# Kernel optimization log

Measured on AMD Instinct MI355X. Metric: run time of the kernel, lower is better.

The kernel has to match this reference:

```python
import jax, jax.numpy as jnp
import numpy as np

B, C, H, W = 16, 128, 64, 64
NH = 8
HD = C // NH          # head dim == pos_embed_dim
WIN = 5               # relative-position window
OUT = 512             # out_dim of the final 1x1 projection


def _dwconv(x, w, pad):
    """Depthwise 2D conv, x: (N, Cin, H, W), w: (Cin, 1, kh, kw)."""
    return jax.lax.conv_general_dilated(
        x, w, window_strides=(1, 1), padding=[(pad, pad), (pad, pad)],
        dimension_numbers=('NCHW', 'OIHW', 'NCHW'),
        feature_group_count=x.shape[1])


def setup_inputs() -> dict:
    key = jax.random.key(0)
    ks = jax.random.split(key, 6)
    src = jax.random.normal(ks[0], (B, C, H, W), jnp.float32)
    cpe_w = jax.random.normal(ks[1], (C, 1, 3, 3), jnp.float32) * 0.1
    qkv_w = jax.random.normal(ks[2], (3 * C, C), jnp.float32) * (1.0 / np.sqrt(C))
    rel_pos = jax.random.normal(ks[3], (HD, WIN, WIN), jnp.float32) * 0.02
    conv1d_w = jax.random.normal(ks[4], (3,), jnp.float32) * 0.5
    out_w = jax.random.normal(ks[5], (OUT, 2 * C), jnp.float32) * (1.0 / np.sqrt(2 * C))
    return dict(src=src, cpe_w=cpe_w, qkv_w=qkv_w, rel_pos=rel_pos,
                conv1d_w=conv1d_w, out_w=out_w)


def reference(src, cpe_w, qkv_w, rel_pos, conv1d_w, out_w):
    scaling = HD ** (-0.5)
    feature_raw = src

    # CPE: depthwise 3x3 conv residual
    s = _dwconv(src, cpe_w, 1) + src

    # 1x1 QKV conv == channel GEMM
    qkv = jnp.einsum('oc,bchw->bohw', qkv_w, s)          # (B, 3C, H, W)
    q, k, v = jnp.split(qkv, 3, axis=1)                  # each (B, C, H, W)

    q = q.reshape(B * NH, HD, H, W)
    k = k.reshape(B * NH, HD, H, W)
    v = v.reshape(B * NH, HD, H, W)

    N = H * W
    kf = jax.nn.softmax(k.reshape(B * NH, HD, N), axis=-1)   # softmax over spatial
    vf = v.reshape(B * NH, HD, N)
    content_lambda = jnp.einsum('bin,bon->bio', kf, vf)      # (B*NH, HD, HD)
    qf = q.reshape(B * NH, HD, N) * scaling
    content_output = jnp.einsum('bin,bio->bon', qf, content_lambda)
    content_output = content_output.reshape(B * NH, HD, H, W)

    # relative-position lambda: depthwise 5x5 conv of v with rel_pos_embed
    position_lambda = _dwconv(v, rel_pos[:, None, :, :], WIN // 2)
    position_output = q * position_lambda

    result1 = (content_output + position_output).reshape(B, C, H, W)

    # ECA-style channel attention on the raw input
    pool = jnp.mean(feature_raw, axis=(2, 3))                # (B, C)
    xp = jnp.pad(pool, ((0, 0), (1, 1)))
    ca = jax.nn.sigmoid(conv1d_w[0] * xp[:, :-2]
                        + conv1d_w[1] * xp[:, 1:-1]
                        + conv1d_w[2] * xp[:, 2:])           # (B, C)
    result2 = feature_raw * ca[:, :, None, None]

    cat = jnp.concatenate([result1, result2], axis=1)       # (B, 2C, H, W)
    return jnp.einsum('oc,bchw->bohw', out_w, cat)           # (B, OUT, H, W)
```

## Files before the change

### kernel.cpp

```cpp
#include <hip/hip_runtime.h>
#include <hip/hip_bf16.h>
#include <math.h>

#define Bb   16
#define Cc   128
#define Hh   64
#define Wwid 64
#define Nn   4096
#define NHh  8
#define HDd  16
#define BHh  128
#define TCc  384
#define OUTc 512
#define KK2  256

typedef _Float16 f16x8 __attribute__((ext_vector_type(8)));
typedef float    f32x4 __attribute__((ext_vector_type(4)));

__device__ __forceinline__ ushort f2h_bits(float f) {
    _Float16 h = (_Float16)f;
    ushort u;
    __builtin_memcpy(&u, &h, 2);
    return u;
}
__device__ __forceinline__ float h2f_bits(ushort u) {
    _Float16 h;
    __builtin_memcpy(&h, &u, 2);
    return (float)h;
}

__global__ void __launch_bounds__(256) cpe_cvt_kernel(
        const float* __restrict__ src, const float* __restrict__ cpe_w,
        const float* __restrict__ qkv_w, const float* __restrict__ out_w,
        ushort* __restrict__ s, float* __restrict__ pool,
        ushort* __restrict__ wq16, ushort* __restrict__ wo16) {
    int t = threadIdx.x;
    if (blockIdx.x >= 2048) {
        int i = (blockIdx.x - 2048) * 256 + t;
        const int na = TCc * Cc, nb = OUTc * KK2;
        if (i < na) wq16[i] = f2h_bits(qkv_w[i]);
        else if (i < na + nb) wo16[i - na] = f2h_bits(out_w[i - na]);
        return;
    }
    int bc = blockIdx.x;
    int c  = bc & (Cc - 1);
    const float* sp = src + (size_t)bc * Nn;
    __shared__ float pl[66 * 66];
    __shared__ float red[256];
    for (int i = t; i < 66 * 66; i += 256) pl[i] = 0.f;
    __syncthreads();
    float lsum = 0.f;
    for (int i = t; i < Nn / 4; i += 256) {
        float4 v4 = ((const float4*)sp)[i];
        lsum += v4.x + v4.y + v4.z + v4.w;
        int e = i * 4, y = e >> 6, x = e & 63;
        float* d = &pl[(y + 1) * 66 + x + 1];
        d[0] = v4.x; d[1] = v4.y; d[2] = v4.z; d[3] = v4.w;
    }
    red[t] = lsum;
    float w[9];
#pragma unroll
    for (int k = 0; k < 9; k++) w[k] = cpe_w[c * 9 + k];
    __syncthreads();
    for (int s2 = 128; s2 > 0; s2 >>= 1) {
        if (t < s2) red[t] += red[t + s2];
        __syncthreads();
    }
    if (t == 0) pool[bc] = red[0] * (1.0f / Nn);
    int x = t & 63, ys = (t >> 6) * 16;
    float r[3][3];
#pragma unroll
    for (int k = 0; k < 2; k++)
#pragma unroll
        for (int j = 0; j < 3; j++) r[k][j] = pl[(ys + k) * 66 + x + j];
    ushort* dst = s + (size_t)bc * Nn;
#pragma unroll
    for (int yy = 0; yy < 16; yy++) {
        int y = ys + yy;
#pragma unroll
        for (int j = 0; j < 3; j++) r[2][j] = pl[(y + 2) * 66 + x + j];
        float acc = r[1][1];
#pragma unroll
        for (int k = 0; k < 3; k++)
#pragma unroll
            for (int j = 0; j < 3; j++) acc += r[k][j] * w[k * 3 + j];
        dst[y * 64 + x] = f2h_bits(acc);
#pragma unroll
        for (int j = 0; j < 3; j++) { r[0][j] = r[1][j]; r[1][j] = r[2][j]; }
    }
}

__global__ void transpose_s(const ushort* __restrict__ s, ushort* __restrict__ sT) {
    int bz = blockIdx.z;
    int c0 = blockIdx.y * 64;
    int n0 = blockIdx.x * 64;
    __shared__ ushort t[64][68];
    int nn = threadIdx.x & 63, c4 = threadIdx.x >> 6;
    const ushort* sp = s + ((size_t)bz * Cc + c0) * Nn + n0;
#pragma unroll
    for (int p = 0; p < 16; p++) {
        int cc = p * 4 + c4;
        t[cc][nn] = sp[(size_t)cc * Nn + nn];
    }
    __syncthreads();
    int cw = threadIdx.x & 63, n4 = threadIdx.x >> 6;
    ushort* dp = sT + ((size_t)bz * Nn + n0) * Cc + c0;
#pragma unroll
    for (int p = 0; p < 16; p++) {
        int n = p * 4 + n4;
        dp[(size_t)n * Cc + cw] = t[cw][n];
    }
}

template<int K, int M, int MODE>
__global__ void __launch_bounds__(256) gemm_tn(const ushort* __restrict__ A,
                                               const ushort* __restrict__ Bt,
                                               float* __restrict__ C,
                                               ushort* __restrict__ q16,
                                               float* __restrict__ kf32,
                                               ushort* __restrict__ v16) {
    const int bz = blockIdx.z;
    const int m0 = blockIdx.y * 128;
    const int n0 = blockIdx.x * 128;
    __shared__ __align__(16) ushort Al[128 * 32];
    __shared__ __align__(16) ushort Bl[128 * 32];
    const int tid  = threadIdx.x;
    const int wave = tid >> 6, lane = tid & 63;
    const int r = lane & 15, q = lane >> 4;
    const int wr = wave >> 1, wc = wave & 1;

    const ushort* Ag = A + (size_t)m0 * K;
    const ushort* Bg = Bt + ((size_t)bz * Nn + n0) * K;

    f32x4 acc[4][4] = {};

    for (int k0 = 0; k0 < K; k0 += 32) {
#pragma unroll
        for (int p = 0; p < 2; p++) {
            int seg = p * 4 + wave;
            int idx = seg * 64 + lane;
            int row = idx >> 2, ch = idx & 3;
            const ushort* ga = Ag + (size_t)row * K + k0 + ch * 8;
            const ushort* gb = Bg + (size_t)row * K + k0 + ch * 8;
            __builtin_amdgcn_global_load_lds(
                (const __attribute__((address_space(1))) void*)(const void*)ga,
                (__attribute__((address_space(3))) void*)(void*)(Al + seg * 512),
                16, 0, 0);
            __builtin_amdgcn_global_load_lds(
                (const __attribute__((address_space(1))) void*)(const void*)gb,
                (__attribute__((address_space(3))) void*)(void*)(Bl + seg * 512),
                16, 0, 0);
        }
        __syncthreads();

        const ushort* Apt = Al + (size_t)(wr * 64 + r) * 32 + q * 8;
        const ushort* Bpt = Bl + (size_t)(wc * 64 + r) * 32 + q * 8;
        f16x8 af[4], bf[4];
#pragma unroll
        for (int i = 0; i < 4; i++) af[i] = *(const f16x8*)(Apt + i * 16 * 32);
#pragma unroll
        for (int j = 0; j < 4; j++) bf[j] = *(const f16x8*)(Bpt + j * 16 * 32);
#pragma unroll
        for (int i = 0; i < 4; i++)
#pragma unroll
            for (int j = 0; j < 4; j++)
                acc[i][j] = __builtin_amdgcn_mfma_f32_16x16x32_f16(af[i], bf[j], acc[i][j], 0, 0, 0);
        __syncthreads();
    }

    if constexpr (MODE == 0) {
        float* Cp = C + ((size_t)bz * M + m0 + wr * 64) * Nn + n0 + wc * 64;
#pragma unroll
        for (int i = 0; i < 4; i++)
#pragma unroll
            for (int j = 0; j < 4; j++)
#pragma unroll
                for (int e = 0; e < 4; e++)
                    Cp[(size_t)(i * 16 + q * 4 + e) * Nn + j * 16 + r] = acc[i][j][e];
    } else {
        size_t base = ((size_t)bz * Cc + wr * 64) * Nn + n0 + wc * 64;
        if (blockIdx.y == 1) {
            float* Cp = kf32 + base;
#pragma unroll
            for (int i = 0; i < 4; i++)
#pragma unroll
                for (int j = 0; j < 4; j++)
#pragma unroll
                    for (int e = 0; e < 4; e++)
                        Cp[(size_t)(i * 16 + q * 4 + e) * Nn + j * 16 + r] = acc[i][j][e];
        } else {
            ushort* Cp = (blockIdx.y == 0 ? q16 : v16) + base;
#pragma unroll
            for (int i = 0; i < 4; i++)
#pragma unroll
                for (int j = 0; j < 4; j++)
#pragma unroll
                    for (int e = 0; e < 4; e++)
                        Cp[(size_t)(i * 16 + q * 4 + e) * Nn + j * 16 + r] = f2h_bits(acc[i][j][e]);
        }
    }
}

__global__ void __launch_bounds__(256) lam_pos_kernel(
        const float* __restrict__ kf32, const ushort* __restrict__ v16,
        const float* __restrict__ rel,
        ushort* __restrict__ pos, float* __restrict__ lamP,
        float* __restrict__ lamE) {
    __shared__ float smem[68 * 68];
    int t = threadIdx.x;

    if (blockIdx.x >= 2048) {
        int bid2 = blockIdx.x - 2048;
        int bh   = bid2 >> 1;
        int half = bid2 & 1;
        int b = bh >> 3, h = bh & 7;
        int wave = t >> 6, lane = t & 63;
        int r = lane & 15, q = lane >> 4;
        const float*  kf = kf32 + ((size_t)b * Cc + h * HDd) * Nn;
        const ushort* vf = v16  + ((size_t)b * Cc + h * HDd) * Nn;

        f32x4 acc = {};
        float esum = 0.f;
        int nbase = half * 2048 + wave * 512;
#pragma unroll 4
        for (int s = 0; s < 16; s++) {
            int n = nbase + s * 32 + q * 8;
            float4 ka = *(const float4*)(kf + (size_t)r * Nn + n);
            float4 kb = *(const float4*)(kf + (size_t)r * Nn + n + 4);
            f16x8 bf = *(const f16x8*)(vf + (size_t)r * Nn + n);
            float e0 = __expf(ka.x), e1 = __expf(ka.y), e2 = __expf(ka.z), e3 = __expf(ka.w);
            float e4 = __expf(kb.x), e5 = __expf(kb.y), e6 = __expf(kb.z), e7 = __expf(kb.w);
            esum += (e0 + e1 + e2 + e3) + (e4 + e5 + e6 + e7);
            f16x8 af;
            af[0] = (_Float16)e0; af[1] = (_Float16)e1;
            af[2] = (_Float16)e2; af[3] = (_Float16)e3;
            af[4] = (_Float16)e4; af[5] = (_Float16)e5;
            af[6] = (_Float16)e6; af[7] = (_Float16)e7;
            acc = __builtin_amdgcn_mfma_f32_16x16x32_f16(af, bf, acc, 0, 0, 0);
        }

        float* red   = smem;
        float* esred = smem + 1024;
#pragma unroll
        for (int e = 0; e < 4; e++) red[wave * 256 + lane * 4 + e] = acc[e];
        esred[wave * 64 + lane] = esum;
        __syncthreads();
        if (wave == 0) {
#pragma unroll
            for (int e = 0; e < 4; e++) {
                float v = red[0 * 256 + lane * 4 + e] + red[1 * 256 + lane * 4 + e]
                        + red[2 * 256 + lane * 4 + e] + red[3 * 256 + lane * 4 + e];
                int row = q * 4 + e;
                lamP[(size_t)half * (BHh * 256) + bh * 256 + row * 16 + r] = v;
            }
            if (lane < 16) {
                float tot = 0.f;
#pragma unroll
                for (int w2 = 0; w2 < 4; w2++)
#pragma unroll
                    for (int qq = 0; qq < 4; qq++)
                        tot += esred[w2 * 64 + qq * 16 + lane];
                lamE[(size_t)half * (BHh * 16) + bh * 16 + lane] = tot;
            }
        }
        return;
    }

    int bc = blockIdx.x;
    int c = bc & (Cc - 1);
    const ushort* vp = v16 + (size_t)bc * Nn;
    float* pl = smem;
    for (int i = t; i < 68 * 68; i += 256) pl[i] = 0.f;
    __syncthreads();
    for (int i = t; i < Nn / 8; i += 256) {
        uint4 u = ((const uint4*)vp)[i];
        ushort us[8]; *(uint4*)us = u;
        int e = i * 8, y = e >> 6, x = e & 63;
        float* d = &pl[(y + 2) * 68 + x + 2];
#pragma unroll
        for (int j = 0; j < 8; j++) d[j] = h2f_bits(us[j]);
    }
    float w[25];
#pragma unroll
    for (int k = 0; k < 25; k++) w[k] = rel[(c & (HDd - 1)) * 25 + k];
    __syncthreads();
    int x = t & 63, ys = (t >> 6) * 16;
    float r[5][5];
#pragma unroll
    for (int k = 0; k < 4; k++)
#pragma unroll
        for (int j = 0; j < 5; j++) r[k][j] = pl[(ys + k) * 68 + x + j];
    ushort* dst = pos + (size_t)bc * Nn;
#pragma unroll
    for (int yy = 0; yy < 16; yy++) {
        int y = ys + yy;
#pragma unroll
        for (int j = 0; j < 5; j++) r[4][j] = pl[(y + 4) * 68 + x + j];
        float acc = 0.f;
#pragma unroll
        for (int k = 0; k < 5; k++)
#pragma unroll
            for (int j = 0; j < 5; j++) acc += r[k][j] * w[k * 5 + j];
        dst[y * 64 + x] = f2h_bits(acc);
#pragma unroll
        for (int k = 0; k < 4; k++)
#pragma unroll
            for (int j = 0; j < 5; j++) r[k][j] = r[k + 1][j];
    }
}

__global__ void __launch_bounds__(256) combine_eca_kernel(
        const ushort* __restrict__ q16, const float* __restrict__ lamP,
        const float* __restrict__ lamE, const ushort* __restrict__ pos,
        const float* __restrict__ src, const float* __restrict__ pool,
        const float* __restrict__ w3, ushort* __restrict__ catT) {
    __shared__ float smem[2240];
    int tid = threadIdx.x;

    if (blockIdx.x >= 2048) {
        int bid2 = blockIdx.x - 2048;
        int n0 = (bid2 & 63) * 64, c0 = ((bid2 >> 6) & 1) * 64, bz = bid2 >> 7;
        ushort* t = (ushort*)smem;
        float* ca_s = smem + 2176;
        if (tid < 64) {
            int c = c0 + tid;
            float left  = (c == 0)        ? 0.f : pool[bz * Cc + c - 1];
            float mid   = pool[bz * Cc + c];
            float right = (c == Cc - 1)   ? 0.f : pool[bz * Cc + c + 1];
            float v = w3[0] * left + w3[1] * mid + w3[2] * right;
            ca_s[tid] = 1.f / (1.f + __expf(-v));
        }
        __syncthreads();
        int nn = tid & 63, c4 = tid >> 6;
        const float* sp = src + ((size_t)bz * Cc + c0) * Nn + n0;
#pragma unroll
        for (int p = 0; p < 16; p++) {
            int cc = p * 4 + c4;
            t[cc * 68 + nn] = f2h_bits(sp[(size_t)cc * Nn + nn] * ca_s[cc]);
        }
        __syncthreads();
        int cw = tid & 63, n4 = tid >> 6;
        ushort* dp = catT + ((size_t)bz * Nn + n0) * KK2 + Cc + c0;
#pragma unroll
        for (int p = 0; p < 16; p++) {
            int n = p * 4 + n4;
            dp[(size_t)n * KK2 + cw] = t[cw * 68 + n];
        }
        return;
    }

    int bh   = blockIdx.x >> 4;
    int tile = blockIdx.x & 15;
    int n = tile * 256 + tid;
    int b = bh >> 3, h = bh & 7;
    float* lam_s = smem;
    {
        int i = tid >> 4;
        float es = lamE[bh * 16 + i] + lamE[(size_t)(BHh * 16) + bh * 16 + i];
        lam_s[tid] = (lamP[bh * 256 + tid]
                    + lamP[(size_t)(BHh * 256) + bh * 256 + tid]) / es;
    }
    __syncthreads();
    const ushort* qp = q16 + ((size_t)b * Cc + h * HDd) * Nn;
    float qv[16];
#pragma unroll
    for (int i = 0; i < 16; i++) qv[i] = h2f_bits(qp[(size_t)i * Nn + n]);
    const ushort* pp = pos + ((size_t)b * Cc + h * HDd) * Nn;
    float vals[16];
#pragma unroll
    for (int o = 0; o < 16; o++) {
        float co = 0.f;
#pragma unroll
        for (int i2 = 0; i2 < 16; i2++) co += qv[i2] * lam_s[i2 * 16 + o];
        vals[o] = co * 0.25f + qv[o] * h2f_bits(pp[(size_t)o * Nn + n]);
    }
    uint up[8];
#pragma unroll
    for (int o2 = 0; o2 < 8; o2++)
        up[o2] = (uint)f2h_bits(vals[2 * o2]) | ((uint)f2h_bits(vals[2 * o2 + 1]) << 16);
    uint4* dst = (uint4*)(catT + ((size_t)b * Nn + n) * KK2 + h * HDd);
    dst[0] = make_uint4(up[0], up[1], up[2], up[3]);
    dst[1] = make_uint4(up[4], up[5], up[6], up[7]);
}

extern "C" void kernel_launch(void* const* d_in, const int* in_sizes, int n_in,
                              void* d_out, int out_size, void* d_ws, size_t ws_size,
                              hipStream_t stream) {
    const float* src      = (const float*)d_in[0];
    const float* cpe_w    = (const float*)d_in[1];
    const float* qkv_w    = (const float*)d_in[2];
    const float* rel_pos  = (const float*)d_in[3];
    const float* conv1d_w = (const float*)d_in[4];
    const float* out_w    = (const float*)d_in[5];
    float* out = (float*)d_out;

    char* ws = (char*)d_ws;
    ushort* q16   = (ushort*)ws;                                 ws += (size_t)Bb * Cc * Nn * 2;
    float*  kf32  = (float*)ws;                                  ws += (size_t)Bb * Cc * Nn * 4;
    ushort* v16   = (ushort*)ws;                                 ws += (size_t)Bb * Cc * Nn * 2;
    ushort* pos   = (ushort*)ws;                                 ws += (size_t)Bb * Cc * Nn * 2;
    ushort* catT  = (ushort*)ws;                                 ws += (size_t)Bb * Nn * KK2 * 2;
    ushort* sT    = (ushort*)ws;                                 ws += (size_t)Bb * Nn * Cc * 2;
    ushort* s16   = (ushort*)catT;
    float*  lamP  = (float*)ws;                                  ws += (size_t)2 * BHh * 256 * 4;
    float*  lamE  = (float*)ws;                                  ws += (size_t)2 * BHh * 16 * 4;
    float*  pool  = (float*)ws;                                  ws += Bb * Cc * 4;
    ushort* wq16  = (ushort*)ws;                                 ws += (size_t)TCc * Cc * 2;
    ushort* wo16  = (ushort*)ws;                                 ws += (size_t)OUTc * KK2 * 2;

    {
        const int nw = TCc * Cc + OUTc * KK2;
        int cvt_blocks = (nw + 255) / 256;
        cpe_cvt_kernel<<<2048 + cvt_blocks, 256, 0, stream>>>(
            src, cpe_w, qkv_w, out_w, s16, pool, wq16, wo16);
    }
    {
        dim3 g(Nn / 64, Cc / 64, Bb);
        transpose_s<<<g, 256, 0, stream>>>(s16, sT);
    }
    {
        dim3 g(Nn / 128, TCc / 128, Bb);
        gemm_tn<Cc, TCc, 1><<<g, 256, 0, stream>>>(wq16, sT, nullptr, q16, kf32, v16);
    }
    lam_pos_kernel<<<2048 + 2 * BHh, 256, 0, stream>>>(kf32, v16, rel_pos, pos, lamP, lamE);
    combine_eca_kernel<<<2048 + 2048, 256, 0, stream>>>(
        q16, lamP, lamE, pos, src, pool, conv1d_w, catT);
    {
        dim3 g(Nn / 128, OUTc / 128, Bb);
        gemm_tn<KK2, OUTc, 0><<<g, 256, 0, stream>>>(wo16, catT, out, nullptr, nullptr, nullptr);
    }
}
```

Before: 268.3 us.

## Double-buffer GEMM LDS tiles, vectorize epilogue via LDS, cache fp16 src

The GEMM mainloop now uses two LDS buffers so the next K-slice is fetched while MFMAs run on the current one, which drops one barrier per iteration. Both GEMM epilogues stage accumulators through a per-wave LDS tile so global stores become float4 or packed-half vectors instead of scattered scalars. The CPE kernel also writes an fp16 copy of src, and the ECA branch reads that copy instead of re-reading fp32 src, which halves its read traffic. The cost is extra LDS per block (possible occupancy loss), an additional fp16 write pass of src, and slightly lower precision on the ECA path.

```diff
diff --git a/kernel.cpp b/kernel.cpp
--- a/kernel.cpp
+++ b/kernel.cpp
@@ -32,7 +32,8 @@
 __global__ void __launch_bounds__(256) cpe_cvt_kernel(
         const float* __restrict__ src, const float* __restrict__ cpe_w,
         const float* __restrict__ qkv_w, const float* __restrict__ out_w,
-        ushort* __restrict__ s, float* __restrict__ pool,
+        ushort* __restrict__ s, ushort* __restrict__ src16,
+        float* __restrict__ pool,
         ushort* __restrict__ wq16, ushort* __restrict__ wo16) {
     int t = threadIdx.x;
     if (blockIdx.x >= 2048) {
@@ -50,9 +51,13 @@
     for (int i = t; i < 66 * 66; i += 256) pl[i] = 0.f;
     __syncthreads();
     float lsum = 0.f;
+    ushort* s16p = src16 + (size_t)bc * Nn;
     for (int i = t; i < Nn / 4; i += 256) {
         float4 v4 = ((const float4*)sp)[i];
         lsum += v4.x + v4.y + v4.z + v4.w;
+        ushort4 h4 = make_ushort4(f2h_bits(v4.x), f2h_bits(v4.y),
+                                  f2h_bits(v4.z), f2h_bits(v4.w));
+        *(ushort4*)(s16p + i * 4) = h4;
         int e = i * 4, y = e >> 6, x = e & 63;
         float* d = &pl[(y + 1) * 66 + x + 1];
         d[0] = v4.x; d[1] = v4.y; d[2] = v4.z; d[3] = v4.w;
@@ -122,8 +127,9 @@
     const int bz = blockIdx.z;
     const int m0 = blockIdx.y * 128;
     const int n0 = blockIdx.x * 128;
-    __shared__ __align__(16) ushort Al[128 * 32];
-    __shared__ __align__(16) ushort Bl[128 * 32];
+    __shared__ __align__(16) ushort Al[2][128 * 32];
+    __shared__ __align__(16) ushort Bl[2][128 * 32];
+    __shared__ __align__(16) float  ep[4][16][66];
     const int tid  = threadIdx.x;
     const int wave = tid >> 6, lane = tid & 63;
     const int r = lane & 15, q = lane >> 4;
@@ -134,7 +140,7 @@
 
     f32x4 acc[4][4] = {};
 
-    for (int k0 = 0; k0 < K; k0 += 32) {
+    auto stage = [&](int buf, int k0) {
 #pragma unroll
         for (int p = 0; p < 2; p++) {
             int seg = p * 4 + wave;
@@ -144,17 +150,25 @@
             const ushort* gb = Bg + (size_t)row * K + k0 + ch * 8;
             __builtin_amdgcn_global_load_lds(
                 (const __attribute__((address_space(1))) void*)(const void*)ga,
-                (__attribute__((address_space(3))) void*)(void*)(Al + seg * 512),
+                (__attribute__((address_space(3))) void*)(void*)(&Al[buf][seg * 512]),
                 16, 0, 0);
             __builtin_amdgcn_global_load_lds(
                 (const __attribute__((address_space(1))) void*)(const void*)gb,
-                (__attribute__((address_space(3))) void*)(void*)(Bl + seg * 512),
+                (__attribute__((address_space(3))) void*)(void*)(&Bl[buf][seg * 512]),
                 16, 0, 0);
         }
-        __syncthreads();
-
-        const ushort* Apt = Al + (size_t)(wr * 64 + r) * 32 + q * 8;
-        const ushort* Bpt = Bl + (size_t)(wc * 64 + r) * 32 + q * 8;
+    };
+
+    constexpr int NT = K / 32;
+    stage(0, 0);
+    __syncthreads();
+#pragma unroll
+    for (int t = 0; t < NT; t++) {
+        const int cur = t & 1;
+        if (t + 1 < NT) stage(cur ^ 1, (t + 1) * 32);
+
+        const ushort* Apt = &Al[cur][(wr * 64 + r) * 32 + q * 8];
+        const ushort* Bpt = &Bl[cur][(wc * 64 + r) * 32 + q * 8];
         f16x8 af[4], bf[4];
 #pragma unroll
         for (int i = 0; i < 4; i++) af[i] = *(const f16x8*)(Apt + i * 16 * 32);
@@ -165,38 +179,62 @@
 #pragma unroll
             for (int j = 0; j < 4; j++)
                 acc[i][j] = __builtin_amdgcn_mfma_f32_16x16x32_f16(af[i], bf[j], acc[i][j], 0, 0, 0);
-        __syncthreads();
+        if (t + 1 < NT) __syncthreads();
     }
 
     if constexpr (MODE == 0) {
         float* Cp = C + ((size_t)bz * M + m0 + wr * 64) * Nn + n0 + wc * 64;
 #pragma unroll
-        for (int i = 0; i < 4; i++)
+        for (int i = 0; i < 4; i++) {
 #pragma unroll
             for (int j = 0; j < 4; j++)
 #pragma unroll
                 for (int e = 0; e < 4; e++)
-                    Cp[(size_t)(i * 16 + q * 4 + e) * Nn + j * 16 + r] = acc[i][j][e];
+                    ep[wave][q * 4 + e][j * 16 + r] = acc[i][j][e];
+#pragma unroll
+            for (int rep = 0; rep < 4; rep++) {
+                int rl = rep * 4 + q;
+                float4 v = *(const float4*)&ep[wave][rl][r * 4];
+                *(float4*)&Cp[(size_t)(i * 16 + rl) * Nn + r * 4] = v;
+            }
+        }
     } else {
         size_t base = ((size_t)bz * Cc + wr * 64) * Nn + n0 + wc * 64;
         if (blockIdx.y == 1) {
             float* Cp = kf32 + base;
 #pragma unroll
-            for (int i = 0; i < 4; i++)
+            for (int i = 0; i < 4; i++) {
 #pragma unroll
                 for (int j = 0; j < 4; j++)
 #pragma unroll
                     for (int e = 0; e < 4; e++)
-                        Cp[(size_t)(i * 16 + q * 4 + e) * Nn + j * 16 + r] = acc[i][j][e];
+                        ep[wave][q * 4 + e][j * 16 + r] = acc[i][j][e];
+#pragma unroll
+                for (int rep = 0; rep < 4; rep++) {
+                    int rl = rep * 4 + q;
+                    float4 v = *(const float4*)&ep[wave][rl][r * 4];
+                    *(float4*)&Cp[(size_t)(i * 16 + rl) * Nn + r * 4] = v;
+                }
+            }
         } else {
             ushort* Cp = (blockIdx.y == 0 ? q16 : v16) + base;
 #pragma unroll
-            for (int i = 0; i < 4; i++)
+            for (int i = 0; i < 4; i++) {
 #pragma unroll
                 for (int j = 0; j < 4; j++)
 #pragma unroll
                     for (int e = 0; e < 4; e++)
-                        Cp[(size_t)(i * 16 + q * 4 + e) * Nn + j * 16 + r] = f2h_bits(acc[i][j][e]);
+                        ep[wave][q * 4 + e][j * 16 + r] = acc[i][j][e];
+#pragma unroll
+                for (int rep = 0; rep < 4; rep++) {
+                    int rl = rep * 4 + q;
+                    float4 v = *(const float4*)&ep[wave][rl][r * 4];
+                    uint2 pk;
+                    pk.x = (uint)f2h_bits(v.x) | ((uint)f2h_bits(v.y) << 16);
+                    pk.y = (uint)f2h_bits(v.z) | ((uint)f2h_bits(v.w) << 16);
+                    *(uint2*)&Cp[(size_t)(i * 16 + rl) * Nn + r * 4] = pk;
+                }
+            }
         }
     }
 }
@@ -312,7 +350,7 @@
 __global__ void __launch_bounds__(256) combine_eca_kernel(
         const ushort* __restrict__ q16, const float* __restrict__ lamP,
         const float* __restrict__ lamE, const ushort* __restrict__ pos,
-        const float* __restrict__ src, const float* __restrict__ pool,
+        const ushort* __restrict__ src16, const float* __restrict__ pool,
         const float* __restrict__ w3, ushort* __restrict__ catT) {
     __shared__ float smem[2240];
     int tid = threadIdx.x;
@@ -332,11 +370,11 @@
         }
         __syncthreads();
         int nn = tid & 63, c4 = tid >> 6;
-        const float* sp = src + ((size_t)bz * Cc + c0) * Nn + n0;
+        const ushort* sp = src16 + ((size_t)bz * Cc + c0) * Nn + n0;
 #pragma unroll
         for (int p = 0; p < 16; p++) {
             int cc = p * 4 + c4;
-            t[cc * 68 + nn] = f2h_bits(sp[(size_t)cc * Nn + nn] * ca_s[cc]);
+            t[cc * 68 + nn] = f2h_bits(h2f_bits(sp[(size_t)cc * Nn + nn]) * ca_s[cc]);
         }
         __syncthreads();
         int cw = tid & 63, n4 = tid >> 6;
@@ -401,6 +439,7 @@
     ushort* pos   = (ushort*)ws;                                 ws += (size_t)Bb * Cc * Nn * 2;
     ushort* catT  = (ushort*)ws;                                 ws += (size_t)Bb * Nn * KK2 * 2;
     ushort* sT    = (ushort*)ws;                                 ws += (size_t)Bb * Nn * Cc * 2;
+    ushort* src16 = (ushort*)ws;                                 ws += (size_t)Bb * Cc * Nn * 2;
     ushort* s16   = (ushort*)catT;
     float*  lamP  = (float*)ws;                                  ws += (size_t)2 * BHh * 256 * 4;
     float*  lamE  = (float*)ws;                                  ws += (size_t)2 * BHh * 16 * 4;
@@ -412,7 +451,7 @@
         const int nw = TCc * Cc + OUTc * KK2;
         int cvt_blocks = (nw + 255) / 256;
         cpe_cvt_kernel<<<2048 + cvt_blocks, 256, 0, stream>>>(
-            src, cpe_w, qkv_w, out_w, s16, pool, wq16, wo16);
+            src, cpe_w, qkv_w, out_w, s16, src16, pool, wq16, wo16);
     }
     {
         dim3 g(Nn / 64, Cc / 64, Bb);
@@ -424,7 +463,7 @@
     }
     lam_pos_kernel<<<2048 + 2 * BHh, 256, 0, stream>>>(kf32, v16, rel_pos, pos, lamP, lamE);
     combine_eca_kernel<<<2048 + 2048, 256, 0, stream>>>(
-        q16, lamP, lamE, pos, src, pool, conv1d_w, catT);
+        q16, lamP, lamE, pos, src16, pool, conv1d_w, catT);
     {
         dim3 g(Nn / 128, OUTc / 128, Bb);
         gemm_tn<KK2, OUTc, 0><<<g, 256, 0, stream>>>(wo16, catT, out, nullptr, nullptr, nullptr);
```

Result: faster. 260.0 us (-3.1%).
